# Kernel optimization log

Hardware: AMD Instinct MI355X
Metric: run time of the kernel (lower is better)

Reference implementation:

```python
import jax, jax.numpy as jnp
import numpy as np

B, H, W = 128, 32, 32
INF = 1e9
EPS = 1e-6  # strictly positive weights -> dist strictly decreases along backtrack (no tie cycles)
OFFS = np.array([(-1, -1), (-1, 0), (-1, 1), (0, -1), (0, 1), (1, -1), (1, 0), (1, 1)], dtype=np.int32)


def _neighbor_min(d):
    # d: [B,H,W] -> per-cell min over 8-neighborhood (INF outside the grid)
    p = jnp.pad(d, ((0, 0), (1, 1), (1, 1)), constant_values=INF)
    sh = jnp.stack([p[:, 1 + dr:1 + dr + H, 1 + dc:1 + dc + W] for dr, dc in OFFS], axis=0)
    return jnp.min(sh, axis=0)


def solve(weights, source, target):
    """Dijkstra/A*(h=0)-equivalent shortest path on an 8-connected grid.
    Entering cell v costs weights[v]; returns a [B,H,W] 0/1 mask of the optimal path
    (source and target cells included). Computed exactly via Bellman-Ford relaxation
    (H*W sweeps >= max hop count) followed by greedy min-dist backtracking.
    """
    w = weights + EPS
    b = jnp.arange(B)
    sr, sc = source[:, 0], source[:, 1]
    ws = w[b, sr, sc]
    dist0 = jnp.full((B, H, W), INF, w.dtype).at[b, sr, sc].set(ws)

    def bf_step(dist, _):
        return jnp.minimum(dist, w + _neighbor_min(dist)), None

    dist, _ = jax.lax.scan(bf_step, dist0, None, length=H * W)

    dist_flat = dist.reshape(B, H * W)
    offs = jnp.asarray(OFFS)  # [8,2]
    hw = jnp.array([H, W], offs.dtype)

    def bt_step(carry, _):
        pos, mask, done = carry            # pos [B,2], mask [B,H,W], done [B]
        r, c = pos[:, 0], pos[:, 1]
        mask = mask.at[b, r, c].max((~done).astype(mask.dtype))
        done = done | ((r == sr) & (c == sc))
        cand = pos[:, None, :] + offs[None]               # [B,8,2]
        valid = ((cand >= 0) & (cand < hw)).all(-1)       # [B,8]
        cr = jnp.clip(cand[..., 0], 0, H - 1)
        cc = jnp.clip(cand[..., 1], 0, W - 1)
        dvals = jnp.take_along_axis(dist_flat, cr * W + cc, axis=1)
        dvals = jnp.where(valid, dvals, INF)
        j = jnp.argmin(dvals, axis=1)                     # predecessor = min-dist neighbor
        nxt = jnp.stack([cr[b, j], cc[b, j]], axis=1)
        pos = jnp.where(done[:, None], pos, nxt)
        return (pos, mask, done), None

    mask0 = jnp.zeros((B, H, W), weights.dtype)
    done0 = jnp.zeros((B,), bool)
    (_, paths, _), _ = jax.lax.scan(bt_step, (target.astype(offs.dtype), mask0, done0), None, length=H * W)
    return paths


def setup_inputs() -> dict:
    key = jax.random.key(0)
    k1, k2, k3 = jax.random.split(key, 3)
    return {
        "weights": jax.random.uniform(k1, (B, H, W), jnp.float32),
        "source": jax.random.randint(k2, (B, 2), 0, H),
        "target": jax.random.randint(k3, (B, 2), 0, H),
    }


def reference(weights, source, target):
    # BBAStar.forward: paths come straight from a_star_batch (the autograd.Function
    # forward is identity on paths); exp_nodes is solver-internal bookkeeping and is
    # not part of the math being differentiated, so we return the path masks.
    return solve(weights, source, target)
```

## Files before the change

kernel.cpp:

```cpp
#include <hip/hip_runtime.h>

#define GH 32
#define GW 32
#define PITCH 34
#define NPAD (PITCH * PITCH)
#define INFV 1000000000.0f
#define EPSV 1e-6f


#define RELAX(i,j) {                                                          \
    const float ul = ((i)==0) ? top[(j)]   : (((j)==0) ? lft[(i)-1] : t[(i)-1][(j)-1]); \
    const float uu = ((i)==0) ? top[(j)+1] : t[(i)-1][(j)];                    \
    const float ur = ((i)==0) ? top[(j)+2] : (((j)==3) ? rgt[(i)-1] : t[(i)-1][(j)+1]); \
    const float ll = ((j)==0) ? lft[(i)]   : t[(i)][(j)-1];                    \
    const float rr = ((j)==3) ? rgt[(i)]   : t[(i)][(j)+1];                    \
    const float dl = ((i)==3) ? bot[(j)]   : (((j)==0) ? lft[(i)+1] : t[(i)+1][(j)-1]); \
    const float dd = ((i)==3) ? bot[(j)+1] : t[(i)+1][(j)];                    \
    const float dr = ((i)==3) ? bot[(j)+2] : (((j)==3) ? rgt[(i)+1] : t[(i)+1][(j)+1]); \
    const float nmin = fminf(fminf(fminf(ul, uu), fminf(ur, ll)),             \
                             fminf(fminf(rr, dl), fminf(dd, dr)));            \
    const float nd = w[i][j] + nmin;                                          \
    if (nd < t[i][j]) { t[i][j] = nd; ch = true; }                            \
}

__global__ __launch_bounds__(64)
void bbastar_kernel(const float* __restrict__ weights,
                    const int* __restrict__ source,
                    const int* __restrict__ target,
                    float* __restrict__ out) {
    __shared__ float d[NPAD];

    const int b   = blockIdx.x;
    const int tid = threadIdx.x;
    const int tr  = tid >> 3;
    const int tc  = tid & 7;
    const int r0  = tr << 2;
    const int c0  = tc << 2;
    const int base = (r0 + 1) * PITCH + (c0 + 1);

    const int sr = source[2 * b];
    const int sc = source[2 * b + 1];

    float w[4][4], t[4][4];
    const float* wb = weights + b * (GH * GW);
    #pragma unroll
    for (int i = 0; i < 4; ++i) {
        const float4 v = *(const float4*)(wb + (r0 + i) * GW + c0);
        w[i][0] = v.x + EPSV; w[i][1] = v.y + EPSV;
        w[i][2] = v.z + EPSV; w[i][3] = v.w + EPSV;
    }

    float4* ob4 = (float4*)(out + b * (GH * GW));
    #pragma unroll
    for (int k = 0; k < 4; ++k) ob4[tid + 64 * k] = make_float4(0.f, 0.f, 0.f, 0.f);

    for (int i = tid; i < NPAD; i += 64) d[i] = INFV;
    #pragma unroll
    for (int i = 0; i < 4; ++i)
        #pragma unroll
        for (int j = 0; j < 4; ++j) t[i][j] = INFV;
    __syncthreads();

    #pragma unroll
    for (int i = 0; i < 4; ++i)
        #pragma unroll
        for (int j = 0; j < 4; ++j)
            if (sr == r0 + i && sc == c0 + j) {
                t[i][j] = w[i][j];
                d[base + i * PITCH + j] = w[i][j];
            }
    __syncthreads();

    for (int it = 0; it < 1024; ++it) {
        float top[6], bot[6], lft[4], rgt[4];
        #pragma unroll
        for (int k = 0; k < 6; ++k) {
            top[k] = d[base - PITCH - 1 + k];
            bot[k] = d[base + 4 * PITCH - 1 + k];
        }
        #pragma unroll
        for (int i = 0; i < 4; ++i) {
            lft[i] = d[base + i * PITCH - 1];
            rgt[i] = d[base + i * PITCH + 4];
        }

        bool ch = false;
        #pragma unroll
        for (int i = 0; i < 4; ++i)
            #pragma unroll
            for (int j = 0; j < 4; ++j) RELAX(i, j)
        #pragma unroll
        for (int i = 3; i >= 0; --i)
            #pragma unroll
            for (int j = 3; j >= 0; --j) RELAX(i, j)

        #pragma unroll
        for (int i = 0; i < 4; ++i)
            #pragma unroll
            for (int j = 0; j < 4; ++j) d[base + i * PITCH + j] = t[i][j];

        const bool any = (__ballot(ch) != 0ULL);
        __syncthreads();
        if (!any) break;
    }

    if (tid == 0) {
        const int drr[8] = {-1, -1, -1,  0, 0,  1, 1, 1};
        const int dcc[8] = {-1,  0,  1, -1, 1, -1, 0, 1};
        int pr = target[2 * b];
        int pc = target[2 * b + 1];
        float* ob = out + b * (GH * GW);
        for (int step = 0; step < GH * GW; ++step) {
            ob[pr * GW + pc] = 1.0f;
            if (pr == sr && pc == sc) break;
            float best = INFV;
            int bj = 0;
            #pragma unroll
            for (int j = 0; j < 8; ++j) {
                const float v = d[(pr + drr[j] + 1) * PITCH + (pc + dcc[j] + 1)];
                if (v < best) { best = v; bj = j; }
            }
            pr += drr[bj];
            pc += dcc[bj];
        }
    }
}

extern "C" void kernel_launch(void* const* d_in, const int* in_sizes, int n_in,
                              void* d_out, int out_size, void* d_ws, size_t ws_size,
                              hipStream_t stream) {
    const float* weights = (const float*)d_in[0];
    const int*   source  = (const int*)d_in[1];
    const int*   target  = (const int*)d_in[2];
    float*       out     = (float*)d_out;
    const int B = in_sizes[0] / (GH * GW);
    bbastar_kernel<<<B, 64, 0, stream>>>(weights, source, target, out);
}
```

Before: 81.09 us.

## Exchange halos via wave shuffles and stop relaxation once target distance is settled

Replaces the per-sweep shared-memory halo exchange and barrier with cross-lane __shfl reads of neighbor tiles within the single 64-thread wavefront. The convergence test becomes Dijkstra-like: the loop exits when no lane changed a value at or below the current target distance, rather than when nothing changed anywhere. Shared memory is written once after convergence for the backtrack, which now checks grid bounds explicitly instead of relying on an INF-padded border. This removes LDS traffic and barriers per sweep and can end sweeps early, at the cost of more shuffle instructions. Cells that are not on the target's optimal path may keep non-final distances, which the greedy backtrack should tolerate since those cells only hold values above the target's.

```diff
diff --git a/kernel.cpp b/kernel.cpp
--- a/kernel.cpp
+++ b/kernel.cpp
@@ -2,8 +2,7 @@
 
 #define GH 32
 #define GW 32
-#define PITCH 34
-#define NPAD (PITCH * PITCH)
+#define P  33
 #define INFV 1000000000.0f
 #define EPSV 1e-6f
 
@@ -20,7 +19,7 @@
     const float nmin = fminf(fminf(fminf(ul, uu), fminf(ur, ll)),             \
                              fminf(fminf(rr, dl), fminf(dd, dr)));            \
     const float nd = w[i][j] + nmin;                                          \
-    if (nd < t[i][j]) { t[i][j] = nd; ch = true; }                            \
+    if (nd < t[i][j]) { t[i][j] = nd; ch = true; chmin = fminf(chmin, nd); }  \
 }
 
 __global__ __launch_bounds__(64)
@@ -28,7 +27,7 @@
                     const int* __restrict__ source,
                     const int* __restrict__ target,
                     float* __restrict__ out) {
-    __shared__ float d[NPAD];
+    __shared__ float d[GH * P];
 
     const int b   = blockIdx.x;
     const int tid = threadIdx.x;
@@ -36,10 +35,11 @@
     const int tc  = tid & 7;
     const int r0  = tr << 2;
     const int c0  = tc << 2;
-    const int base = (r0 + 1) * PITCH + (c0 + 1);
 
-    const int sr = source[2 * b];
-    const int sc = source[2 * b + 1];
+    const int sr  = source[2 * b];
+    const int sc  = source[2 * b + 1];
+    const int tgr = target[2 * b];
+    const int tgc = target[2 * b + 1];
 
     float w[4][4], t[4][4];
     const float* wb = weights + b * (GH * GW);
@@ -54,37 +54,50 @@
     #pragma unroll
     for (int k = 0; k < 4; ++k) ob4[tid + 64 * k] = make_float4(0.f, 0.f, 0.f, 0.f);
 
-    for (int i = tid; i < NPAD; i += 64) d[i] = INFV;
     #pragma unroll
     for (int i = 0; i < 4; ++i)
         #pragma unroll
         for (int j = 0; j < 4; ++j) t[i][j] = INFV;
-    __syncthreads();
-
     #pragma unroll
     for (int i = 0; i < 4; ++i)
         #pragma unroll
         for (int j = 0; j < 4; ++j)
-            if (sr == r0 + i && sc == c0 + j) {
-                t[i][j] = w[i][j];
-                d[base + i * PITCH + j] = w[i][j];
-            }
-    __syncthreads();
+            if (sr == r0 + i && sc == c0 + j) t[i][j] = w[i][j];
 
-    for (int it = 0; it < 1024; ++it) {
+    const int  tl = ((tgr >> 2) << 3) | (tgc >> 2);
+    const int  ti = tgr & 3;
+    const int  tj = tgc & 3;
+    const bool hu = tr > 0, hd = tr < 7, hl = tc > 0, hr = tc < 7;
+
+    for (int sweep = 0; sweep < 8192; ++sweep) {
         float top[6], bot[6], lft[4], rgt[4];
         #pragma unroll
-        for (int k = 0; k < 6; ++k) {
-            top[k] = d[base - PITCH - 1 + k];
-            bot[k] = d[base + 4 * PITCH - 1 + k];
+        for (int j = 0; j < 4; ++j) {
+            const float su = __shfl(t[3][j], (tid - 8) & 63);
+            const float sd = __shfl(t[0][j], (tid + 8) & 63);
+            top[j + 1] = hu ? su : INFV;
+            bot[j + 1] = hd ? sd : INFV;
+        }
+        {
+            const float s_tl = __shfl(t[3][3], (tid - 9) & 63);
+            const float s_tr = __shfl(t[3][0], (tid - 7) & 63);
+            const float s_bl = __shfl(t[0][3], (tid + 7) & 63);
+            const float s_br = __shfl(t[0][0], (tid + 9) & 63);
+            top[0] = (hu && hl) ? s_tl : INFV;
+            top[5] = (hu && hr) ? s_tr : INFV;
+            bot[0] = (hd && hl) ? s_bl : INFV;
+            bot[5] = (hd && hr) ? s_br : INFV;
         }
         #pragma unroll
         for (int i = 0; i < 4; ++i) {
-            lft[i] = d[base + i * PITCH - 1];
-            rgt[i] = d[base + i * PITCH + 4];
+            const float sl = __shfl(t[i][3], (tid - 1) & 63);
+            const float sr2 = __shfl(t[i][0], (tid + 1) & 63);
+            lft[i] = hl ? sl : INFV;
+            rgt[i] = hr ? sr2 : INFV;
         }
 
         bool ch = false;
+        float chmin = INFV;
         #pragma unroll
         for (int i = 0; i < 4; ++i)
             #pragma unroll
@@ -94,21 +107,30 @@
             #pragma unroll
             for (int j = 3; j >= 0; --j) RELAX(i, j)
 
+        float tv = t[0][0];
         #pragma unroll
         for (int i = 0; i < 4; ++i)
             #pragma unroll
-            for (int j = 0; j < 4; ++j) d[base + i * PITCH + j] = t[i][j];
+            for (int j = 0; j < 4; ++j)
+                if (ti == i && tj == j) tv = t[i][j];
+        const float dtgt = __shfl(tv, tl);
 
-        const bool any = (__ballot(ch) != 0ULL);
-        __syncthreads();
-        if (!any) break;
+        const bool pred = ch && (chmin <= dtgt);
+        if (__ballot(pred) == 0ULL) break;
     }
+
+    #pragma unroll
+    for (int i = 0; i < 4; ++i)
+        #pragma unroll
+        for (int j = 0; j < 4; ++j)
+            d[(r0 + i) * P + (c0 + j)] = t[i][j];
+    __syncthreads();
 
     if (tid == 0) {
         const int drr[8] = {-1, -1, -1,  0, 0,  1, 1, 1};
         const int dcc[8] = {-1,  0,  1, -1, 1, -1, 0, 1};
-        int pr = target[2 * b];
-        int pc = target[2 * b + 1];
+        int pr = tgr;
+        int pc = tgc;
         float* ob = out + b * (GH * GW);
         for (int step = 0; step < GH * GW; ++step) {
             ob[pr * GW + pc] = 1.0f;
@@ -117,8 +139,12 @@
             int bj = 0;
             #pragma unroll
             for (int j = 0; j < 8; ++j) {
-                const float v = d[(pr + drr[j] + 1) * PITCH + (pc + dcc[j] + 1)];
-                if (v < best) { best = v; bj = j; }
+                const int nr = pr + drr[j], nc = pc + dcc[j];
+                const bool ok = (nr >= 0) & (nr < GH) & (nc >= 0) & (nc < GW);
+                const int cr = min(max(nr, 0), GH - 1);
+                const int cc = min(max(nc, 0), GW - 1);
+                const float vv = ok ? d[cr * P + cc] : INFV;
+                if (vv < best) { best = vv; bj = j; }
             }
             pr += drr[bj];
             pc += dcc[bj];
```

After: 91.81 us. 13.2% more time.

## Exchange tile borders after each sweep direction and write only border cells

Applied to the files above, without the earlier changes.

Each iteration now does a forward sweep, publishes the tile border to LDS, syncs, rereads the halo, then does a backward sweep and publishes again. Before, both sweeps ran on the same halo with one exchange per iteration. Each exchange now writes only the 12 border cells, and the full interior is written once after convergence for the backtrack. The relaxation is made branchless with fminf, and the change flag is tracked only in the backward sweep. The intent is faster propagation between tiles, so fewer outer iterations are needed, at the cost of an extra barrier and halo read per iteration.

```diff
diff --git a/kernel.cpp b/kernel.cpp
--- a/kernel.cpp
+++ b/kernel.cpp
@@ -2,13 +2,16 @@
 
 #define GH 32
 #define GW 32
-#define PITCH 34
-#define NPAD (PITCH * PITCH)
+#define P  34
+#define NP (P * P)
 #define INFV 1000000000.0f
 #define EPSV 1e-6f
 
 
-#define RELAX(i,j) {                                                          \
+#define NMIN8(ul,uu,ur,ll,rr,dl,dd,dr) \
+    fminf(fminf(fminf(fminf((ul),(uu)),(ur)), fminf(fminf((ll),(rr)),(dl))), fminf((dd),(dr)))
+
+#define RELAXF(i,j) {                                                         \
     const float ul = ((i)==0) ? top[(j)]   : (((j)==0) ? lft[(i)-1] : t[(i)-1][(j)-1]); \
     const float uu = ((i)==0) ? top[(j)+1] : t[(i)-1][(j)];                    \
     const float ur = ((i)==0) ? top[(j)+2] : (((j)==3) ? rgt[(i)-1] : t[(i)-1][(j)+1]); \
@@ -17,10 +20,47 @@
     const float dl = ((i)==3) ? bot[(j)]   : (((j)==0) ? lft[(i)+1] : t[(i)+1][(j)-1]); \
     const float dd = ((i)==3) ? bot[(j)+1] : t[(i)+1][(j)];                    \
     const float dr = ((i)==3) ? bot[(j)+2] : (((j)==3) ? rgt[(i)+1] : t[(i)+1][(j)+1]); \
-    const float nmin = fminf(fminf(fminf(ul, uu), fminf(ur, ll)),             \
-                             fminf(fminf(rr, dl), fminf(dd, dr)));            \
-    const float nd = w[i][j] + nmin;                                          \
-    if (nd < t[i][j]) { t[i][j] = nd; ch = true; }                            \
+    const float nd = w[i][j] + NMIN8(ul,uu,ur,ll,rr,dl,dd,dr);                \
+    t[i][j] = fminf(t[i][j], nd);                                             \
+}
+
+#define RELAXB(i,j) {                                                         \
+    const float ul = ((i)==0) ? top[(j)]   : (((j)==0) ? lft[(i)-1] : t[(i)-1][(j)-1]); \
+    const float uu = ((i)==0) ? top[(j)+1] : t[(i)-1][(j)];                    \
+    const float ur = ((i)==0) ? top[(j)+2] : (((j)==3) ? rgt[(i)-1] : t[(i)-1][(j)+1]); \
+    const float ll = ((j)==0) ? lft[(i)]   : t[(i)][(j)-1];                    \
+    const float rr = ((j)==3) ? rgt[(i)]   : t[(i)][(j)+1];                    \
+    const float dl = ((i)==3) ? bot[(j)]   : (((j)==0) ? lft[(i)+1] : t[(i)+1][(j)-1]); \
+    const float dd = ((i)==3) ? bot[(j)+1] : t[(i)+1][(j)];                    \
+    const float dr = ((i)==3) ? bot[(j)+2] : (((j)==3) ? rgt[(i)+1] : t[(i)+1][(j)+1]); \
+    const float nd = w[i][j] + NMIN8(ul,uu,ur,ll,rr,dl,dd,dr);                \
+    ch = ch || (nd < t[i][j]);                                                \
+    t[i][j] = fminf(t[i][j], nd);                                             \
+}
+
+#define RINGREAD {                                                            \
+    _Pragma("unroll")                                                         \
+    for (int k = 0; k < 6; ++k) {                                             \
+        top[k] = d[base - P - 1 + k];                                         \
+        bot[k] = d[base + 4 * P - 1 + k];                                     \
+    }                                                                         \
+    _Pragma("unroll")                                                         \
+    for (int i = 0; i < 4; ++i) {                                             \
+        lft[i] = d[base + i * P - 1];                                         \
+        rgt[i] = d[base + i * P + 4];                                         \
+    }                                                                         \
+}
+
+#define BORDERWRITE {                                                         \
+    _Pragma("unroll")                                                         \
+    for (int j = 0; j < 4; ++j) {                                             \
+        d[base + j]         = t[0][j];                                        \
+        d[base + 3 * P + j] = t[3][j];                                        \
+    }                                                                         \
+    d[base + P]         = t[1][0];                                            \
+    d[base + 2 * P]     = t[2][0];                                            \
+    d[base + P + 3]     = t[1][3];                                            \
+    d[base + 2 * P + 3] = t[2][3];                                            \
 }
 
 __global__ __launch_bounds__(64)
@@ -28,7 +68,7 @@
                     const int* __restrict__ source,
                     const int* __restrict__ target,
                     float* __restrict__ out) {
-    __shared__ float d[NPAD];
+    __shared__ float d[NP];
 
     const int b   = blockIdx.x;
     const int tid = threadIdx.x;
@@ -36,10 +76,10 @@
     const int tc  = tid & 7;
     const int r0  = tr << 2;
     const int c0  = tc << 2;
-    const int base = (r0 + 1) * PITCH + (c0 + 1);
+    const int base = (r0 + 1) * P + (c0 + 1);
 
-    const int sr = source[2 * b];
-    const int sc = source[2 * b + 1];
+    const int sr  = source[2 * b];
+    const int sc  = source[2 * b + 1];
 
     float w[4][4], t[4][4];
     const float* wb = weights + b * (GH * GW);
@@ -54,7 +94,7 @@
     #pragma unroll
     for (int k = 0; k < 4; ++k) ob4[tid + 64 * k] = make_float4(0.f, 0.f, 0.f, 0.f);
 
-    for (int i = tid; i < NPAD; i += 64) d[i] = INFV;
+    for (int i = tid; i < NP; i += 64) d[i] = INFV;
     #pragma unroll
     for (int i = 0; i < 4; ++i)
         #pragma unroll
@@ -67,42 +107,37 @@
         for (int j = 0; j < 4; ++j)
             if (sr == r0 + i && sc == c0 + j) {
                 t[i][j] = w[i][j];
-                d[base + i * PITCH + j] = w[i][j];
+                d[base + i * P + j] = w[i][j];
             }
     __syncthreads();
 
-    for (int it = 0; it < 1024; ++it) {
-        float top[6], bot[6], lft[4], rgt[4];
-        #pragma unroll
-        for (int k = 0; k < 6; ++k) {
-            top[k] = d[base - PITCH - 1 + k];
-            bot[k] = d[base + 4 * PITCH - 1 + k];
-        }
-        #pragma unroll
-        for (int i = 0; i < 4; ++i) {
-            lft[i] = d[base + i * PITCH - 1];
-            rgt[i] = d[base + i * PITCH + 4];
-        }
-
-        bool ch = false;
+    float top[6], bot[6], lft[4], rgt[4];
+    for (int pair = 0; pair < 2048; ++pair) {
+        RINGREAD
         #pragma unroll
         for (int i = 0; i < 4; ++i)
             #pragma unroll
-            for (int j = 0; j < 4; ++j) RELAX(i, j)
+            for (int j = 0; j < 4; ++j) RELAXF(i, j)
+        BORDERWRITE
+        __syncthreads();
+
+        RINGREAD
+        bool ch = false;
         #pragma unroll
         for (int i = 3; i >= 0; --i)
             #pragma unroll
-            for (int j = 3; j >= 0; --j) RELAX(i, j)
+            for (int j = 3; j >= 0; --j) RELAXB(i, j)
+        BORDERWRITE
+        __syncthreads();
+        if (__ballot(ch) == 0ULL) break;
+    }
 
+    #pragma unroll
+    for (int i = 0; i < 4; ++i)
         #pragma unroll
-        for (int i = 0; i < 4; ++i)
-            #pragma unroll
-            for (int j = 0; j < 4; ++j) d[base + i * PITCH + j] = t[i][j];
-
-        const bool any = (__ballot(ch) != 0ULL);
-        __syncthreads();
-        if (!any) break;
-    }
+        for (int j = 0; j < 4; ++j)
+            d[base + i * P + j] = t[i][j];
+    __syncthreads();
 
     if (tid == 0) {
         const int drr[8] = {-1, -1, -1,  0, 0,  1, 1, 1};
@@ -117,8 +152,8 @@
             int bj = 0;
             #pragma unroll
             for (int j = 0; j < 8; ++j) {
-                const float v = d[(pr + drr[j] + 1) * PITCH + (pc + dcc[j] + 1)];
-                if (v < best) { best = v; bj = j; }
+                const float vv = d[(pr + drr[j] + 1) * P + (pc + dcc[j] + 1)];
+                if (vv < best) { best = vv; bj = j; }
             }
             pr += drr[bj];
             pc += dcc[bj];
```

After: 76.35 us. 1.06x faster.

## Alternate four directional sweep units per sync with boundary-only shared writes

Applied to the files above, without the earlier changes.

Replaces the forward-plus-backward raster pass per iteration with a cycle of four single-pass sweeps: row-forward, column-forward, row-backward, column-backward. Each sweep syncs and checks convergence, so values cross tile boundaries more often per unit of relaxation work. Each sweep writes only the tile's ring cells to shared memory, and the full tile is flushed after convergence. Ring loads use float2 and the update is branchless. The trade-off is more barriers and ballots per cell update, and fewer relaxations done between exchanges.

```diff
diff --git a/kernel.cpp b/kernel.cpp
--- a/kernel.cpp
+++ b/kernel.cpp
@@ -2,13 +2,16 @@
 
 #define GH 32
 #define GW 32
-#define PITCH 34
-#define NPAD (PITCH * PITCH)
+#define P  34
+#define NP (P * P)
 #define INFV 1000000000.0f
 #define EPSV 1e-6f
 
 
-#define RELAX(i,j) {                                                          \
+#define NMIN8(ul,uu,ur,ll,rr,dl,dd,dr) \
+    fminf(fminf(fminf(fminf((ul),(uu)),(ur)), fminf(fminf((ll),(rr)),(dl))), fminf((dd),(dr)))
+
+#define RELAXC(i,j) {                                                         \
     const float ul = ((i)==0) ? top[(j)]   : (((j)==0) ? lft[(i)-1] : t[(i)-1][(j)-1]); \
     const float uu = ((i)==0) ? top[(j)+1] : t[(i)-1][(j)];                    \
     const float ur = ((i)==0) ? top[(j)+2] : (((j)==3) ? rgt[(i)-1] : t[(i)-1][(j)+1]); \
@@ -17,18 +20,61 @@
     const float dl = ((i)==3) ? bot[(j)]   : (((j)==0) ? lft[(i)+1] : t[(i)+1][(j)-1]); \
     const float dd = ((i)==3) ? bot[(j)+1] : t[(i)+1][(j)];                    \
     const float dr = ((i)==3) ? bot[(j)+2] : (((j)==3) ? rgt[(i)+1] : t[(i)+1][(j)+1]); \
-    const float nmin = fminf(fminf(fminf(ul, uu), fminf(ur, ll)),             \
-                             fminf(fminf(rr, dl), fminf(dd, dr)));            \
-    const float nd = w[i][j] + nmin;                                          \
-    if (nd < t[i][j]) { t[i][j] = nd; ch = true; }                            \
+    const float old = t[(i)][(j)];                                            \
+    const float nd  = w[(i)][(j)] + NMIN8(ul,uu,ur,ll,rr,dl,dd,dr);           \
+    ch = ch || (nd < old);                                                    \
+    t[(i)][(j)] = fminf(old, nd);                                             \
 }
+
+#define RINGREAD {                                                            \
+    const float2 t0 = *(const float2*)&d[base - P - 1];                       \
+    const float2 t1 = *(const float2*)&d[base - P + 1];                       \
+    const float2 t2 = *(const float2*)&d[base - P + 3];                       \
+    top[0]=t0.x; top[1]=t0.y; top[2]=t1.x; top[3]=t1.y; top[4]=t2.x; top[5]=t2.y; \
+    const float2 b0 = *(const float2*)&d[base + 4*P - 1];                     \
+    const float2 b1 = *(const float2*)&d[base + 4*P + 1];                     \
+    const float2 b2 = *(const float2*)&d[base + 4*P + 3];                     \
+    bot[0]=b0.x; bot[1]=b0.y; bot[2]=b1.x; bot[3]=b1.y; bot[4]=b2.x; bot[5]=b2.y; \
+    lft[0]=d[base-1];     lft[1]=d[base+P-1];   lft[2]=d[base+2*P-1]; lft[3]=d[base+3*P-1]; \
+    rgt[0]=d[base+4];     rgt[1]=d[base+P+4];   rgt[2]=d[base+2*P+4]; rgt[3]=d[base+3*P+4]; \
+}
+
+#define WR(i,j) d[base + (i)*P + (j)] = t[i][j];
+
+#define UNIT_ROWF { float top[6], bot[6], lft[4], rgt[4]; RINGREAD bool ch=false; \
+  RELAXC(0,0) RELAXC(0,1) RELAXC(0,2) RELAXC(0,3) WR(0,0) WR(0,1) WR(0,2) WR(0,3) \
+  RELAXC(1,0) RELAXC(1,1) RELAXC(1,2) RELAXC(1,3) WR(1,0) WR(1,3)                 \
+  RELAXC(2,0) RELAXC(2,1) RELAXC(2,2) RELAXC(2,3) WR(2,0) WR(2,3)                 \
+  RELAXC(3,0) RELAXC(3,1) RELAXC(3,2) RELAXC(3,3) WR(3,0) WR(3,1) WR(3,2) WR(3,3) \
+  __syncthreads(); if (__ballot(ch) == 0ULL) goto relax_done; }
+
+#define UNIT_COLF { float top[6], bot[6], lft[4], rgt[4]; RINGREAD bool ch=false; \
+  RELAXC(0,0) RELAXC(1,0) RELAXC(2,0) RELAXC(3,0) WR(0,0) WR(1,0) WR(2,0) WR(3,0) \
+  RELAXC(0,1) RELAXC(1,1) RELAXC(2,1) RELAXC(3,1) WR(0,1) WR(3,1)                 \
+  RELAXC(0,2) RELAXC(1,2) RELAXC(2,2) RELAXC(3,2) WR(0,2) WR(3,2)                 \
+  RELAXC(0,3) RELAXC(1,3) RELAXC(2,3) RELAXC(3,3) WR(0,3) WR(1,3) WR(2,3) WR(3,3) \
+  __syncthreads(); if (__ballot(ch) == 0ULL) goto relax_done; }
+
+#define UNIT_ROWB { float top[6], bot[6], lft[4], rgt[4]; RINGREAD bool ch=false; \
+  RELAXC(3,3) RELAXC(3,2) RELAXC(3,1) RELAXC(3,0) WR(3,3) WR(3,2) WR(3,1) WR(3,0) \
+  RELAXC(2,3) RELAXC(2,2) RELAXC(2,1) RELAXC(2,0) WR(2,3) WR(2,0)                 \
+  RELAXC(1,3) RELAXC(1,2) RELAXC(1,1) RELAXC(1,0) WR(1,3) WR(1,0)                 \
+  RELAXC(0,3) RELAXC(0,2) RELAXC(0,1) RELAXC(0,0) WR(0,3) WR(0,2) WR(0,1) WR(0,0) \
+  __syncthreads(); if (__ballot(ch) == 0ULL) goto relax_done; }
+
+#define UNIT_COLB { float top[6], bot[6], lft[4], rgt[4]; RINGREAD bool ch=false; \
+  RELAXC(3,3) RELAXC(2,3) RELAXC(1,3) RELAXC(0,3) WR(3,3) WR(2,3) WR(1,3) WR(0,3) \
+  RELAXC(3,2) RELAXC(2,2) RELAXC(1,2) RELAXC(0,2) WR(3,2) WR(0,2)                 \
+  RELAXC(3,1) RELAXC(2,1) RELAXC(1,1) RELAXC(0,1) WR(3,1) WR(0,1)                 \
+  RELAXC(3,0) RELAXC(2,0) RELAXC(1,0) RELAXC(0,0) WR(3,0) WR(2,0) WR(1,0) WR(0,0) \
+  __syncthreads(); if (__ballot(ch) == 0ULL) goto relax_done; }
 
 __global__ __launch_bounds__(64)
 void bbastar_kernel(const float* __restrict__ weights,
                     const int* __restrict__ source,
                     const int* __restrict__ target,
                     float* __restrict__ out) {
-    __shared__ float d[NPAD];
+    __shared__ alignas(16) float d[NP];
 
     const int b   = blockIdx.x;
     const int tid = threadIdx.x;
@@ -36,10 +82,10 @@
     const int tc  = tid & 7;
     const int r0  = tr << 2;
     const int c0  = tc << 2;
-    const int base = (r0 + 1) * PITCH + (c0 + 1);
+    const int base = (r0 + 1) * P + (c0 + 1);
 
-    const int sr = source[2 * b];
-    const int sc = source[2 * b + 1];
+    const int sr  = source[2 * b];
+    const int sc  = source[2 * b + 1];
 
     float w[4][4], t[4][4];
     const float* wb = weights + b * (GH * GW);
@@ -54,7 +100,12 @@
     #pragma unroll
     for (int k = 0; k < 4; ++k) ob4[tid + 64 * k] = make_float4(0.f, 0.f, 0.f, 0.f);
 
-    for (int i = tid; i < NPAD; i += 64) d[i] = INFV;
+    {
+        float4* d4 = (float4*)d;
+        #pragma unroll
+        for (int i = tid; i < NP / 4; i += 64)
+            d4[i] = make_float4(INFV, INFV, INFV, INFV);
+    }
     #pragma unroll
     for (int i = 0; i < 4; ++i)
         #pragma unroll
@@ -67,42 +118,24 @@
         for (int j = 0; j < 4; ++j)
             if (sr == r0 + i && sc == c0 + j) {
                 t[i][j] = w[i][j];
-                d[base + i * PITCH + j] = w[i][j];
+                d[base + i * P + j] = w[i][j];
             }
     __syncthreads();
 
-    for (int it = 0; it < 1024; ++it) {
-        float top[6], bot[6], lft[4], rgt[4];
+    for (int cyc = 0; cyc < 1024; ++cyc) {
+        UNIT_ROWF
+        UNIT_COLF
+        UNIT_ROWB
+        UNIT_COLB
+    }
+relax_done: ;
+
+    #pragma unroll
+    for (int i = 0; i < 4; ++i)
         #pragma unroll
-        for (int k = 0; k < 6; ++k) {
-            top[k] = d[base - PITCH - 1 + k];
-            bot[k] = d[base + 4 * PITCH - 1 + k];
-        }
-        #pragma unroll
-        for (int i = 0; i < 4; ++i) {
-            lft[i] = d[base + i * PITCH - 1];
-            rgt[i] = d[base + i * PITCH + 4];
-        }
-
-        bool ch = false;
-        #pragma unroll
-        for (int i = 0; i < 4; ++i)
-            #pragma unroll
-            for (int j = 0; j < 4; ++j) RELAX(i, j)
-        #pragma unroll
-        for (int i = 3; i >= 0; --i)
-            #pragma unroll
-            for (int j = 3; j >= 0; --j) RELAX(i, j)
-
-        #pragma unroll
-        for (int i = 0; i < 4; ++i)
-            #pragma unroll
-            for (int j = 0; j < 4; ++j) d[base + i * PITCH + j] = t[i][j];
-
-        const bool any = (__ballot(ch) != 0ULL);
-        __syncthreads();
-        if (!any) break;
-    }
+        for (int j = 0; j < 4; ++j)
+            d[base + i * P + j] = t[i][j];
+    __syncthreads();
 
     if (tid == 0) {
         const int drr[8] = {-1, -1, -1,  0, 0,  1, 1, 1};
@@ -117,8 +150,8 @@
             int bj = 0;
             #pragma unroll
             for (int j = 0; j < 8; ++j) {
-                const float v = d[(pr + drr[j] + 1) * PITCH + (pc + dcc[j] + 1)];
-                if (v < best) { best = v; bj = j; }
+                const float vv = d[(pr + drr[j] + 1) * P + (pc + dcc[j] + 1)];
+                if (vv < best) { best = vv; bj = j; }
             }
             pr += drr[bj];
             pc += dcc[bj];
```

New measurement: 77.68 us. -4.2%, faster.
